# Optimization experiments

Measured on AMD Instinct MI355X. Metric: run time of the kernel, lower is better.

The kernel has to match this reference:

```python
import jax, jax.numpy as jnp
import numpy as np

N_BLOCKS = 1_000_000
N_FILES = 10_000
DIM = 128


def setup_inputs() -> dict:
    key = jax.random.key(0)
    k1, k2, k3, k4, k5 = jax.random.split(key, 5)
    h_blk = jax.random.normal(k1, (N_BLOCKS, DIM), dtype=jnp.float32)
    interior = jnp.sort(jax.random.randint(k2, (N_FILES - 1,), 0, N_BLOCKS))
    blk_ptr = jnp.concatenate([jnp.zeros((1,), jnp.int32), interior.astype(jnp.int32), jnp.full((1,), N_BLOCKS, jnp.int32)])
    # learned params: nn.Linear(dim, dim) weight/bias + context vector
    W = jax.random.normal(k3, (DIM, DIM), dtype=jnp.float32) / np.sqrt(DIM)
    b = jax.random.normal(k4, (DIM,), dtype=jnp.float32) * 0.01
    context = jax.random.normal(k5, (DIM,), dtype=jnp.float32)
    return {"h_blk": h_blk, "W": W, "b": b, "context": context, "blk_ptr": blk_ptr}


def reference(h_blk, W, b, context, blk_ptr):
    N = h_blk.shape[0]
    B = blk_ptr.shape[0] - 1  # static number of segments
    # segment id for each block row: row i in [blk_ptr[k], blk_ptr[k+1]) -> k
    seg = jnp.searchsorted(blk_ptr[1:], jnp.arange(N), side="right")
    # scores = tanh(h @ W^T + b) @ context  -> [N]
    scores = jnp.tanh(h_blk @ W.T + b) @ context
    # per-segment stable softmax
    seg_max = jax.ops.segment_max(scores, seg, num_segments=B)
    e = jnp.exp(scores - seg_max[seg])
    denom = jax.ops.segment_sum(e, seg, num_segments=B)
    alpha = e / denom[seg]
    # weighted sum per segment -> [B, dim]; empty segments give zero rows
    h_file = jax.ops.segment_sum(alpha[:, None] * h_blk, seg, num_segments=B)
    return h_file, alpha
```

## Files before the change

kernel.cpp:

```cpp
#include <hip/hip_runtime.h>
#include <stdint.h>


typedef __attribute__((ext_vector_type(8))) short short8;
typedef __attribute__((ext_vector_type(4))) float f32x4;

#define DIM 128
#define MAXL 4096
#define WPAD 136

struct __align__(16) SMemA {
  unsigned short W[128 * WPAD];
  unsigned short h[4][16 * WPAD];
  float bias[DIM];
  float ctx[DIM];
};

__device__ inline unsigned short f2b(float f) {
  union { float f; uint32_t i; } v; v.f = f;
  uint32_t r = v.i + 0x7FFFu + ((v.i >> 16) & 1u);
  return (unsigned short)(r >> 16);
}
__device__ inline float tanh_fast(float x) {
  float e2 = __expf(2.0f * x);
  return 1.0f - 2.0f * __builtin_amdgcn_rcpf(e2 + 1.0f);
}

__global__ __launch_bounds__(256, 3) void scores_kernel(
    const float* __restrict__ h_blk,
    const float* __restrict__ Wg,
    const float* __restrict__ bg,
    const float* __restrict__ cg,
    float* __restrict__ e_out,
    int N)
{
  __shared__ SMemA sm;
  const int tid  = threadIdx.x;
  const int wave = tid >> 6;
  const int lane = tid & 63;

  {
    const float4* Wg4 = (const float4*)Wg;
    for (int rep = 0; rep < 16; ++rep) {
      int c = rep * 256 + tid;
      int row  = c >> 5;
      int col4 = (c & 31) * 4;
      float4 v = Wg4[c];
      ushort4 o;
      o.x = f2b(v.x); o.y = f2b(v.y); o.z = f2b(v.z); o.w = f2b(v.w);
      *(ushort4*)&sm.W[row * WPAD + col4] = o;
    }
    if (tid < DIM) { sm.bias[tid] = bg[tid]; sm.ctx[tid] = cg[tid]; }
  }
  __syncthreads();

  const int quad = lane >> 4;
  const int mrow = lane & 15;
  const int ntiles = (N + 15) >> 4;
  const int gw = blockIdx.x * 4 + wave;
  const int nw = gridDim.x * 4;
  const float4* hg4 = (const float4*)h_blk;
  unsigned short* ht = sm.h[wave];

  for (int t = gw; t < ntiles; t += nw) {
    const int tb = t * 16;
    const int rows = min(16, N - tb);

    for (int rep = 0; rep < 8; ++rep) {
      int c = rep * 64 + lane;
      int row  = c >> 5;
      int col4 = (c & 31) * 4;
      float4 v = make_float4(0.f, 0.f, 0.f, 0.f);
      if (row < rows) v = hg4[(size_t)(tb + row) * 32 + (c & 31)];
      ushort4 o;
      o.x = f2b(v.x); o.y = f2b(v.y); o.z = f2b(v.z); o.w = f2b(v.w);
      *(ushort4*)&ht[row * WPAD + col4] = o;
    }

    const unsigned short* ar = &ht[mrow * WPAD + quad * 8];
    short8 a0 = *(const short8*)&ar[0];
    short8 a1 = *(const short8*)&ar[32];
    short8 a2 = *(const short8*)&ar[64];
    short8 a3 = *(const short8*)&ar[96];

    float part0 = 0.f, part1 = 0.f, part2 = 0.f, part3 = 0.f;
    for (int nt = 0; nt < 8; ++nt) {
      const unsigned short* wr = &sm.W[(nt * 16 + mrow) * WPAD + quad * 8];
      short8 b0 = *(const short8*)&wr[0];
      short8 b1 = *(const short8*)&wr[32];
      short8 b2 = *(const short8*)&wr[64];
      short8 b3 = *(const short8*)&wr[96];
      f32x4 c = {0.f, 0.f, 0.f, 0.f};
      c = __builtin_amdgcn_mfma_f32_16x16x32_bf16(a0, b0, c, 0, 0, 0);
      c = __builtin_amdgcn_mfma_f32_16x16x32_bf16(a1, b1, c, 0, 0, 0);
      c = __builtin_amdgcn_mfma_f32_16x16x32_bf16(a2, b2, c, 0, 0, 0);
      c = __builtin_amdgcn_mfma_f32_16x16x32_bf16(a3, b3, c, 0, 0, 0);
      float bj = sm.bias[nt * 16 + mrow];
      float cj = sm.ctx[nt * 16 + mrow];
      part0 += tanh_fast(c.x + bj) * cj;
      part1 += tanh_fast(c.y + bj) * cj;
      part2 += tanh_fast(c.z + bj) * cj;
      part3 += tanh_fast(c.w + bj) * cj;
    }
    for (int m = 1; m <= 8; m <<= 1) {
      part0 += __shfl_xor(part0, m);
      part1 += __shfl_xor(part1, m);
      part2 += __shfl_xor(part2, m);
      part3 += __shfl_xor(part3, m);
    }
    float e0 = __expf(fminf(part0, 87.f)), e1 = __expf(fminf(part1, 87.f));
    float e2 = __expf(fminf(part2, 87.f)), e3 = __expf(fminf(part3, 87.f));
    if (mrow == 0) {
      int rb = quad * 4;
      if (rows == 16) {
        *(float4*)&e_out[tb + rb] = make_float4(e0, e1, e2, e3);
      } else {
        if (rb + 0 < rows) e_out[tb + rb + 0] = e0;
        if (rb + 1 < rows) e_out[tb + rb + 1] = e1;
        if (rb + 2 < rows) e_out[tb + rb + 2] = e2;
        if (rb + 3 < rows) e_out[tb + rb + 3] = e3;
      }
    }
  }
}

__global__ __launch_bounds__(256, 4) void pool_kernel(
    const float* __restrict__ h_blk,
    const int* __restrict__ blk_ptr,
    float* __restrict__ h_file,
    float* __restrict__ e_alpha)
{
  __shared__ float se[MAXL];
  __shared__ float red[4][DIM];
  __shared__ float dn[4];

  const int tid  = threadIdx.x;
  const int wave = tid >> 6;
  const int lane = tid & 63;
  const int seg  = blockIdx.x;
  const int r0 = blk_ptr[seg];
  const int r1 = blk_ptr[seg + 1];
  int L = r1 - r0;
  if (L > MAXL) L = MAXL;

  float ds = 0.f;
  for (int i = tid; i < L; i += 256) {
    float v = e_alpha[r0 + i];
    se[i] = v;
    ds += v;
  }
  for (int m = 1; m <= 32; m <<= 1) ds += __shfl_xor(ds, m);
  if (lane == 0) dn[wave] = ds;
  __syncthreads();

  const float D = dn[0] + dn[1] + dn[2] + dn[3];
  const float rD = (D > 0.f) ? (1.0f / D) : 0.f;

  const int half = lane >> 5;
  const int dq   = lane & 31;
  float4 acc = make_float4(0.f, 0.f, 0.f, 0.f);
  for (int base = wave * 8; base < L; base += 32) {
#pragma unroll
    for (int u = 0; u < 4; ++u) {
      int i = base + u * 2 + half;
      if (i < L) {
        float ei = se[i];
        float4 hv = *(const float4*)&h_blk[(size_t)(r0 + i) * DIM + dq * 4];
        acc.x += ei * hv.x; acc.y += ei * hv.y;
        acc.z += ei * hv.z; acc.w += ei * hv.w;
      }
    }
  }
  acc.x += __shfl_xor(acc.x, 32);
  acc.y += __shfl_xor(acc.y, 32);
  acc.z += __shfl_xor(acc.z, 32);
  acc.w += __shfl_xor(acc.w, 32);
  if (half == 0) *(float4*)&red[wave][dq * 4] = acc;

  for (int i = tid; i < L; i += 256) {
    e_alpha[r0 + i] = se[i] * rD;
  }
  __syncthreads();

  if (tid < DIM) {
    float s = red[0][tid] + red[1][tid] + red[2][tid] + red[3][tid];
    h_file[(size_t)seg * DIM + tid] = s * rD;
  }
}

extern "C" void kernel_launch(void* const* d_in, const int* in_sizes, int n_in,
                              void* d_out, int out_size, void* d_ws, size_t ws_size,
                              hipStream_t stream) {
  const float* h_blk = (const float*)d_in[0];
  const float* Wg    = (const float*)d_in[1];
  const float* bg    = (const float*)d_in[2];
  const float* cg    = (const float*)d_in[3];
  const int*   bp    = (const int*)d_in[4];
  const int N = in_sizes[0] / DIM;
  const int B = in_sizes[4] - 1;

  float* out    = (float*)d_out;
  float* h_file = out;
  float* alpha  = out + (size_t)B * DIM;

  scores_kernel<<<dim3(768), dim3(256), 0, stream>>>(h_blk, Wg, bg, cg, alpha, N);
  pool_kernel<<<dim3(B), dim3(256), 0, stream>>>(h_blk, bp, h_file, alpha);
}
```

Measured before the change: 804.8 us.

## Fuse segment pooling into scores kernel with atomics and register prefetch

Pooling is folded into the scores pass. Each wave now walks a contiguous range of 16-row tiles, finds its starting segment by binary search, and accumulates the exp-weighted sum from the bf16 tile already staged in LDS. It flushes partial numerators and denominators to global memory with atomics at segment boundaries. A zero kernel clears the outputs first, and a small finalize kernel divides h_file and alpha by the denominator. The aim is to avoid reading h_blk a second time; the costs are atomic contention, a serial per-row loop, and pooling done on bf16-rounded inputs, which lowers precision.

```diff
diff --git a/kernel.cpp b/kernel.cpp
--- a/kernel.cpp
+++ b/kernel.cpp
@@ -6,7 +6,6 @@
 typedef __attribute__((ext_vector_type(4))) float f32x4;
 
 #define DIM 128
-#define MAXL 4096
 #define WPAD 136
 
 struct __align__(16) SMemA {
@@ -14,6 +13,7 @@
   unsigned short h[4][16 * WPAD];
   float bias[DIM];
   float ctx[DIM];
+  float e[4][16];
 };
 
 __device__ inline unsigned short f2b(float f) {
@@ -24,6 +24,19 @@
 __device__ inline float tanh_fast(float x) {
   float e2 = __expf(2.0f * x);
   return 1.0f - 2.0f * __builtin_amdgcn_rcpf(e2 + 1.0f);
+}
+__device__ inline void atomic_add_f32(float* p, float v) {
+  __hip_atomic_fetch_add(p, v, __ATOMIC_RELAXED, __HIP_MEMORY_SCOPE_AGENT);
+}
+
+__global__ void zero_kernel(float* __restrict__ hf, float* __restrict__ Dg,
+                            int n_hf, int n_d) {
+  int i = (blockIdx.x * 256 + threadIdx.x) * 4;
+  if (i < n_hf) *(float4*)&hf[i] = make_float4(0.f, 0.f, 0.f, 0.f);
+  if (i < n_d) {
+    if (i + 3 < n_d) *(float4*)&Dg[i] = make_float4(0.f, 0.f, 0.f, 0.f);
+    else for (int k = i; k < n_d; ++k) Dg[k] = 0.f;
+  }
 }
 
 __global__ __launch_bounds__(256, 3) void scores_kernel(
@@ -31,8 +44,11 @@
     const float* __restrict__ Wg,
     const float* __restrict__ bg,
     const float* __restrict__ cg,
+    const int* __restrict__ bp,
     float* __restrict__ e_out,
-    int N)
+    float* __restrict__ h_file,
+    float* __restrict__ Dg,
+    int N, int B)
 {
   __shared__ SMemA sm;
   const int tid  = threadIdx.x;
@@ -59,22 +75,70 @@
   const int ntiles = (N + 15) >> 4;
   const int gw = blockIdx.x * 4 + wave;
   const int nw = gridDim.x * 4;
+  const int cpw = (ntiles + nw - 1) / nw;
+  const int t0 = gw * cpw;
+  const int t1 = min(t0 + cpw, ntiles);
+  if (t0 >= t1) return;
+
   const float4* hg4 = (const float4*)h_blk;
   unsigned short* ht = sm.h[wave];
-
-  for (int t = gw; t < ntiles; t += nw) {
-    const int tb = t * 16;
+  float* ebuf = sm.e[wave];
+
+  int cur, nxt;
+  {
+    int r0r = t0 << 4;
+    int lo = 0, hi = B;
+    while (hi - lo > 1) {
+      int mid = (lo + hi) >> 1;
+      if (bp[mid] <= r0r) lo = mid; else hi = mid;
+    }
+    cur = lo; nxt = bp[lo + 1];
+  }
+
+  float num0 = 0.f, num1 = 0.f, dsum = 0.f;
+  const int j0 = lane * 2;
+
+  auto flush = [&]() {
+    atomic_add_f32(&h_file[(size_t)cur * DIM + j0],     num0);
+    atomic_add_f32(&h_file[(size_t)cur * DIM + j0 + 1], num1);
+    if (lane == 0) atomic_add_f32(&Dg[cur], dsum);
+    num0 = num1 = dsum = 0.f;
+  };
+
+  float4 v[8];
+  {
+    int tb = t0 << 4; int rows = min(16, N - tb);
+#pragma unroll
+    for (int rep = 0; rep < 8; ++rep) {
+      int c = rep * 64 + lane; int row = c >> 5;
+      v[rep] = (row < rows) ? hg4[(size_t)(tb + row) * 32 + (c & 31)]
+                            : make_float4(0.f, 0.f, 0.f, 0.f);
+    }
+  }
+
+  for (int t = t0; t < t1; ++t) {
+    const int tb = t << 4;
     const int rows = min(16, N - tb);
 
+#pragma unroll
     for (int rep = 0; rep < 8; ++rep) {
       int c = rep * 64 + lane;
       int row  = c >> 5;
       int col4 = (c & 31) * 4;
-      float4 v = make_float4(0.f, 0.f, 0.f, 0.f);
-      if (row < rows) v = hg4[(size_t)(tb + row) * 32 + (c & 31)];
       ushort4 o;
-      o.x = f2b(v.x); o.y = f2b(v.y); o.z = f2b(v.z); o.w = f2b(v.w);
+      o.x = f2b(v[rep].x); o.y = f2b(v[rep].y);
+      o.z = f2b(v[rep].z); o.w = f2b(v[rep].w);
       *(ushort4*)&ht[row * WPAD + col4] = o;
+    }
+
+    if (t + 1 < t1) {
+      int tb2 = (t + 1) << 4; int rows2 = min(16, N - tb2);
+#pragma unroll
+      for (int rep = 0; rep < 8; ++rep) {
+        int c = rep * 64 + lane; int row = c >> 5;
+        v[rep] = (row < rows2) ? hg4[(size_t)(tb2 + row) * 32 + (c & 31)]
+                               : make_float4(0.f, 0.f, 0.f, 0.f);
+      }
     }
 
     const unsigned short* ar = &ht[mrow * WPAD + quad * 8];
@@ -120,71 +184,40 @@
         if (rb + 2 < rows) e_out[tb + rb + 2] = e2;
         if (rb + 3 < rows) e_out[tb + rb + 3] = e3;
       }
-    }
-  }
-}
-
-__global__ __launch_bounds__(256, 4) void pool_kernel(
-    const float* __restrict__ h_blk,
-    const int* __restrict__ blk_ptr,
+      *(float4*)&ebuf[rb] = make_float4(e0, e1, e2, e3);
+    }
+
+    for (int i = 0; i < rows; ++i) {
+      int r = tb + i;
+      if (r >= nxt) {
+        flush();
+        do { ++cur; nxt = bp[cur + 1]; } while (nxt <= r);
+      }
+      float ei = ebuf[i];
+      uint32_t u = *(const uint32_t*)&ht[i * WPAD + j0];
+      num0 += ei * __uint_as_float(u << 16);
+      num1 += ei * __uint_as_float(u & 0xFFFF0000u);
+      dsum += ei;
+    }
+  }
+  flush();
+}
+
+__global__ __launch_bounds__(128) void finalize_kernel(
+    const int* __restrict__ bp,
+    const float* __restrict__ Dg,
     float* __restrict__ h_file,
     float* __restrict__ e_alpha)
 {
-  __shared__ float se[MAXL];
-  __shared__ float red[4][DIM];
-  __shared__ float dn[4];
-
-  const int tid  = threadIdx.x;
-  const int wave = tid >> 6;
-  const int lane = tid & 63;
-  const int seg  = blockIdx.x;
-  const int r0 = blk_ptr[seg];
-  const int r1 = blk_ptr[seg + 1];
-  int L = r1 - r0;
-  if (L > MAXL) L = MAXL;
-
-  float ds = 0.f;
-  for (int i = tid; i < L; i += 256) {
-    float v = e_alpha[r0 + i];
-    se[i] = v;
-    ds += v;
-  }
-  for (int m = 1; m <= 32; m <<= 1) ds += __shfl_xor(ds, m);
-  if (lane == 0) dn[wave] = ds;
-  __syncthreads();
-
-  const float D = dn[0] + dn[1] + dn[2] + dn[3];
+  const int seg = blockIdx.x;
+  const int tid = threadIdx.x;
+  const float D = Dg[seg];
   const float rD = (D > 0.f) ? (1.0f / D) : 0.f;
-
-  const int half = lane >> 5;
-  const int dq   = lane & 31;
-  float4 acc = make_float4(0.f, 0.f, 0.f, 0.f);
-  for (int base = wave * 8; base < L; base += 32) {
-#pragma unroll
-    for (int u = 0; u < 4; ++u) {
-      int i = base + u * 2 + half;
-      if (i < L) {
-        float ei = se[i];
-        float4 hv = *(const float4*)&h_blk[(size_t)(r0 + i) * DIM + dq * 4];
-        acc.x += ei * hv.x; acc.y += ei * hv.y;
-        acc.z += ei * hv.z; acc.w += ei * hv.w;
-      }
-    }
-  }
-  acc.x += __shfl_xor(acc.x, 32);
-  acc.y += __shfl_xor(acc.y, 32);
-  acc.z += __shfl_xor(acc.z, 32);
-  acc.w += __shfl_xor(acc.w, 32);
-  if (half == 0) *(float4*)&red[wave][dq * 4] = acc;
-
-  for (int i = tid; i < L; i += 256) {
-    e_alpha[r0 + i] = se[i] * rD;
-  }
-  __syncthreads();
-
-  if (tid < DIM) {
-    float s = red[0][tid] + red[1][tid] + red[2][tid] + red[3][tid];
-    h_file[(size_t)seg * DIM + tid] = s * rD;
+  h_file[(size_t)seg * DIM + tid] *= rD;
+  const int r0 = bp[seg];
+  const int r1 = bp[seg + 1];
+  for (int i = r0 + tid; i < r1; i += 128) {
+    e_alpha[i] *= rD;
   }
 }
 
@@ -202,7 +235,12 @@
   float* out    = (float*)d_out;
   float* h_file = out;
   float* alpha  = out + (size_t)B * DIM;
-
-  scores_kernel<<<dim3(768), dim3(256), 0, stream>>>(h_blk, Wg, bg, cg, alpha, N);
-  pool_kernel<<<dim3(B), dim3(256), 0, stream>>>(h_blk, bp, h_file, alpha);
-}
+  float* Dg     = (float*)d_ws;
+
+  const int n_hf = B * DIM;
+  const int zero_blocks = (n_hf / 4 + 255) / 256;
+  zero_kernel<<<dim3(zero_blocks), dim3(256), 0, stream>>>(h_file, Dg, n_hf, B);
+  scores_kernel<<<dim3(768), dim3(256), 0, stream>>>(h_blk, Wg, bg, cg, bp,
+                                                     alpha, h_file, Dg, N, B);
+  finalize_kernel<<<dim3(B), dim3(128), 0, stream>>>(bp, Dg, h_file, alpha);
+}
```

Measured after the change: 700.5 us. 13.0% less time.
